# Kernel tuning notes

Hardware: AMD Instinct MI355X
Metric: run time of the kernel (lower is better)

Reference implementation:

```python
import jax, jax.numpy as jnp
import numpy as np

T = 1.0        # temperature (init kwarg t)
NEG = -1e9     # finite mask value: exp(NEG - max) underflows to exactly 0 in fp32


def setup_inputs() -> dict:
    key = jax.random.key(0)
    k1, k2 = jax.random.split(key)
    B, L, D = 48, 17, 256
    x = jax.random.normal(k1, (B, L, D), dtype=jnp.float32)
    label = jax.random.randint(k2, (B,), 0, 8, dtype=jnp.int64)
    return {"input": x, "label": label}


def _loss(x, label):
    B, L, D = x.shape
    M = B * (L - 1)
    # F.normalize(dim=2)
    xn = x / jnp.maximum(jnp.linalg.norm(x, axis=2, keepdims=True), 1e-12)
    anchors = xn[:, 0]                         # [B, D]
    toks = xn[:, 1:].reshape(M, D)             # [M, D], row r belongs to sample owner[r]
    owner = jnp.repeat(jnp.arange(B), L - 1)   # [M]
    same = label[:, None] == label[owner][None, :]   # [B, M] same-class mask per anchor
    neg = ~same                                      # negative-column mask per anchor

    s_anc = (anchors @ toks.T) / T   # [B, M] anchor-vs-token scores
    s_tok = (toks @ toks.T) / T      # [M, M] token-vs-token scores

    # anchor_consistent_score_unify: softmax of s_anc over negative columns only
    a_logits = jnp.where(neg, s_anc, NEG)                       # [B, M]
    log_denom = jax.scipy.special.logsumexp(a_logits, axis=1)   # [B]  log sum_c exp(s_anc)
    a_unify = jnp.exp(a_logits - log_denom[:, None])            # [B, M], 0 at masked cols
    # positive_consistent_score_unify: exp(s_tok) / anchor denom (NOT a row softmax)
    p_unify = jnp.exp(s_tok[None, :, :] - log_denom[:, None, None])  # [B, M, M]

    # second-level Softmax / LogSoftmax applied to the unify VALUES, neg cols only
    a_m = jnp.where(neg, a_unify, NEG)                 # [B, M]
    p_m = jnp.where(neg[:, None, :], p_unify, NEG)     # [B, M, M]
    log_a = jax.nn.log_softmax(a_m, axis=1)            # [B, M]
    log_p = jax.nn.log_softmax(p_m, axis=2)            # [B, M, M]
    sm_a = jnp.exp(log_a)
    sm_p = jnp.exp(log_p)

    col = neg[:, None, :]
    # KL(input=log_a repeated over rows, target=sm_p), elementwise t*(log t - inp)
    kl1 = jnp.where(col, sm_p * (log_p - log_a[:, None, :]), 0.0).sum(axis=2)          # [B, M]
    # KL(input=log_p, target=sm_a repeated over rows)
    kl2 = jnp.where(col, sm_a[:, None, :] * (log_a[:, None, :] - log_p), 0.0).sum(axis=2)

    row = same.astype(x.dtype)              # positive rows for anchor i
    P = row.sum(axis=1)                     # batchmean divisor = #positive rows
    l1 = (kl1 * row).sum(axis=1) / P
    l2 = (kl2 * row).sum(axis=1) / P
    return jnp.mean(0.5 * l1 + 0.5 * l2)


def reference(input, label):
    return _loss(input, label)
```

## Files before the change

### kernel.cpp

```cpp
#include <hip/hip_runtime.h>
#include <math.h>

#define Bn 48
#define Ln 17
#define Dn 256
#define Mn 768
#define NS 2
#define LDA 76

static __device__ __forceinline__ double pexp(double e) {
  return 1.0 + e*(1.0 + e*(0.5 + e*((1.0/6.0) + e*((1.0/24.0) + e*(1.0/120.0)))));
}

static __device__ __forceinline__ double blockReduce16(double v, double* red) {
  __syncthreads();
  #pragma unroll
  for (int o = 32; o > 0; o >>= 1) v += __shfl_down(v, o, 64);
  int lane = threadIdx.x & 63, wid = threadIdx.x >> 6;
  if (lane == 0) red[wid] = v;
  __syncthreads();
  double r = 0.0;
  #pragma unroll
  for (int w = 0; w < 16; ++w) r += red[w];
  return r;
}

static __device__ __forceinline__ int src_row_m(int m) {
  if (m < Bn) return m * Ln;
  int t = m - Bn;
  return (t >> 4) * Ln + (t & 15) + 1;
}
static __device__ __forceinline__ int src_row_n(int n) {
  return (n >> 4) * Ln + (n & 15) + 1;
}

__global__ __launch_bounds__(256) void kA_gemm(const float* __restrict__ x,
                                               double* __restrict__ EA,
                                               double* __restrict__ E,
                                               float* __restrict__ out) {
  __shared__ float As[16][LDA];
  __shared__ float Bs[16][LDA];
  __shared__ float nA[64], nB[64];
  int tid = threadIdx.x;
  if (blockIdx.x == 0 && blockIdx.y == 0 && tid == 0) out[0] = 0.f;
  int m0 = blockIdx.y * 64, n0 = blockIdx.x * 64;
  int r  = tid >> 2, cq = tid & 3;
  int mrow = m0 + r;
  int gm = (mrow < 816) ? src_row_m(mrow) : 0;
  int gn = src_row_n(n0 + r);
  const float* pa = x + gm * Dn + cq * 4;
  const float* pb = x + gn * Dn + cq * 4;
  float4 ra = *(const float4*)pa;
  float4 rb = *(const float4*)pb;
  float ssa = 0.f, ssb = 0.f;
  float c[4][4];
  #pragma unroll
  for (int i = 0; i < 4; ++i)
    #pragma unroll
    for (int j = 0; j < 4; ++j) c[i][j] = 0.f;
  int tx = tid & 15, ty = tid >> 4;

  for (int t = 0; t < 16; ++t) {
    __syncthreads();
    int kb = cq * 4;
    As[kb+0][r] = ra.x; As[kb+1][r] = ra.y; As[kb+2][r] = ra.z; As[kb+3][r] = ra.w;
    Bs[kb+0][r] = rb.x; Bs[kb+1][r] = rb.y; Bs[kb+2][r] = rb.z; Bs[kb+3][r] = rb.w;
    ssa += ra.x*ra.x + ra.y*ra.y + ra.z*ra.z + ra.w*ra.w;
    ssb += rb.x*rb.x + rb.y*rb.y + rb.z*rb.z + rb.w*rb.w;
    __syncthreads();
    if (t < 15) {
      ra = *(const float4*)(pa + (t + 1) * 16);
      rb = *(const float4*)(pb + (t + 1) * 16);
    }
    #pragma unroll
    for (int k = 0; k < 16; ++k) {
      float4 a4 = *(const float4*)&As[k][ty * 4];
      float4 b4 = *(const float4*)&Bs[k][tx * 4];
      float av[4] = {a4.x, a4.y, a4.z, a4.w};
      float bv[4] = {b4.x, b4.y, b4.z, b4.w};
      #pragma unroll
      for (int i = 0; i < 4; ++i)
        #pragma unroll
        for (int j = 0; j < 4; ++j) c[i][j] = fmaf(av[i], bv[j], c[i][j]);
    }
  }
  ssa += __shfl_xor(ssa, 1, 64); ssa += __shfl_xor(ssa, 2, 64);
  ssb += __shfl_xor(ssb, 1, 64); ssb += __shfl_xor(ssb, 2, 64);
  if (cq == 0) { nA[r] = ssa; nB[r] = ssb; }
  __syncthreads();
  double ia[4], ib[4];
  #pragma unroll
  for (int i = 0; i < 4; ++i) ia[i] = 1.0 / sqrt((double)nA[ty * 4 + i]);
  #pragma unroll
  for (int j = 0; j < 4; ++j) ib[j] = 1.0 / sqrt((double)nB[tx * 4 + j]);
  #pragma unroll
  for (int i = 0; i < 4; ++i) {
    int m = m0 + ty * 4 + i;
    if (m >= 816) continue;
    #pragma unroll
    for (int j = 0; j < 4; ++j) {
      int n = n0 + tx * 4 + j;
      double ev = exp((double)c[i][j] * ia[i] * ib[j]);
      if (m < Bn) EA[m * Mn + n] = ev;
      else        E[(m - Bn) * Mn + n] = ev;
    }
  }
}

__global__ __launch_bounds__(1024, 2) void kB_i(const double* __restrict__ EA,
                                                const double* __restrict__ E,
                                                const int* __restrict__ label,
                                                float* __restrict__ out) {
  __shared__ double2 sp[Mn];
  __shared__ double red[16];
  __shared__ int lab[Bn];
  int slice = blockIdx.x, i = blockIdx.y;
  int tid = threadIdx.x;
  int lane = tid & 63, w = tid >> 6;
  if (tid < Bn) lab[tid] = label[tid];
  __syncthreads();
  int li = lab[i];

  bool has = (tid < Mn);
  bool neg = has && (lab[tid >> 4] != li);
  double eav = has ? EA[i * Mn + tid] : 0.0;
  double s1 = blockReduce16(neg ? eav : 0.0, red);
  double ci = 1.0 / s1;
  double a = ci * eav;
  double p = pexp(a);
  if (has) { sp[tid].x = neg ? a : 0.0; sp[tid].y = neg ? p : 0.0; }
  double t2a = blockReduce16(neg ? p : 0.0, red);
  double t2b = blockReduce16(neg ? p * a : 0.0, red);
  double inv_s2 = 1.0 / t2a;
  double Evi = t2b * inv_s2;
  unsigned long long nm = __ballot(lane < Bn && lab[lane] != li);
  int cnt = 64 - __popcll(nm | 0xFFFF000000000000ull);

  int kb0 = lane >> 4;
  double tsum = 0.0;
  for (int bj = slice; bj < Bn; bj += NS) {
    if (lab[bj] != li) continue;
    const double* Ej = E + (bj * 16 + w) * Mn + lane;
    double Evv[12];
    #pragma unroll
    for (int it = 0; it < 12; ++it) Evv[it] = Ej[64 * it];
    double A = 0.0, Bv = 0.0, C = 0.0, D2 = 0.0;
    #pragma unroll
    for (int it = 0; it < 12; ++it) {
      double m = (double)((nm >> (kb0 + 4 * it)) & 1ull);
      double e = ci * Evv[it];
      double wx = pexp(e);
      double wm = wx * m;
      double2 s = sp[lane + 64 * it];
      A  = fma(wm, e, A);
      Bv = fma(wx, s.x, Bv);
      C += wm;
      D2 = fma(s.y, e, D2);
    }
    #pragma unroll
    for (int o = 32; o > 0; o >>= 1) {
      A  += __shfl_xor(A,  o, 64);
      Bv += __shfl_xor(Bv, o, 64);
      C  += __shfl_xor(C,  o, 64);
      D2 += __shfl_xor(D2, o, 64);
    }
    tsum += (A - Bv) / C - D2 * inv_s2 + Evi;
  }

  __syncthreads();
  if (lane == 0) red[w] = tsum;
  __syncthreads();
  if (tid == 0) {
    double s = 0.0;
    #pragma unroll
    for (int ww = 0; ww < 16; ++ww) s += red[ww];
    atomicAdd(out, (float)(s / (1536.0 * (double)cnt)));
  }
}

extern "C" void kernel_launch(void* const* d_in, const int* in_sizes, int n_in,
                              void* d_out, int out_size, void* d_ws, size_t ws_size,
                              hipStream_t stream) {
  const float* x   = (const float*)d_in[0];
  const int* label = (const int*)d_in[1];
  float* out = (float*)d_out;

  char* ws = (char*)d_ws;
  size_t off = 0;
  auto alloc = [&](size_t bytes) -> void* {
    void* p = ws + off;
    off = (off + bytes + 255) & ~(size_t)255;
    return p;
  };
  double* EA = (double*)alloc((size_t)Bn * Mn * sizeof(double));
  double* E  = (double*)alloc((size_t)Mn * Mn * sizeof(double));

  kA_gemm<<<dim3(12, 13), 256, 0, stream>>>(x, EA, E, out);
  kB_i<<<dim3(NS, Bn), 1024, 0, stream>>>(EA, E, label, out);
}
```

Baseline: 91.92 us.

## Fuse GEMM and loss kernels into one cooperative launch with grid sync

Merges the score/exp GEMM kernel and the per-anchor KL reduction kernel into a single cooperative kernel of 1024-thread blocks. A grid-wide sync separates the two phases, and only the first 96 blocks continue into the reduction. The GEMM phase now gives each thread a 2x2 output tile, but only 256 threads do the loads. This removes one kernel launch and its inter-kernel gap. The cost is a grid barrier, a smaller per-thread tile, idle loader threads, and a reduction phase that may run at lower occupancy.

```diff
diff --git a/kernel.cpp b/kernel.cpp
--- a/kernel.cpp
+++ b/kernel.cpp
@@ -1,12 +1,16 @@
 #include <hip/hip_runtime.h>
+#include <hip/hip_cooperative_groups.h>
 #include <math.h>
+
+namespace cg = cooperative_groups;
 
 #define Bn 48
 #define Ln 17
 #define Dn 256
 #define Mn 768
-#define NS 2
 #define LDA 76
+#define NBLK 156
+#define NKB 96
 
 static __device__ __forceinline__ double pexp(double e) {
   return 1.0 + e*(1.0 + e*(0.5 + e*((1.0/6.0) + e*((1.0/24.0) + e*(1.0/120.0)))));
@@ -34,88 +38,100 @@
   return (n >> 4) * Ln + (n & 15) + 1;
 }
 
-__global__ __launch_bounds__(256) void kA_gemm(const float* __restrict__ x,
+__global__ __launch_bounds__(1024) void kFused(const float* __restrict__ x,
+                                               const int* __restrict__ label,
                                                double* __restrict__ EA,
                                                double* __restrict__ E,
                                                float* __restrict__ out) {
-  __shared__ float As[16][LDA];
-  __shared__ float Bs[16][LDA];
-  __shared__ float nA[64], nB[64];
-  int tid = threadIdx.x;
-  if (blockIdx.x == 0 && blockIdx.y == 0 && tid == 0) out[0] = 0.f;
-  int m0 = blockIdx.y * 64, n0 = blockIdx.x * 64;
-  int r  = tid >> 2, cq = tid & 3;
-  int mrow = m0 + r;
-  int gm = (mrow < 816) ? src_row_m(mrow) : 0;
-  int gn = src_row_n(n0 + r);
-  const float* pa = x + gm * Dn + cq * 4;
-  const float* pb = x + gn * Dn + cq * 4;
-  float4 ra = *(const float4*)pa;
-  float4 rb = *(const float4*)pb;
-  float ssa = 0.f, ssb = 0.f;
-  float c[4][4];
-  #pragma unroll
-  for (int i = 0; i < 4; ++i)
-    #pragma unroll
-    for (int j = 0; j < 4; ++j) c[i][j] = 0.f;
-  int tx = tid & 15, ty = tid >> 4;
-
-  for (int t = 0; t < 16; ++t) {
-    __syncthreads();
-    int kb = cq * 4;
-    As[kb+0][r] = ra.x; As[kb+1][r] = ra.y; As[kb+2][r] = ra.z; As[kb+3][r] = ra.w;
-    Bs[kb+0][r] = rb.x; Bs[kb+1][r] = rb.y; Bs[kb+2][r] = rb.z; Bs[kb+3][r] = rb.w;
-    ssa += ra.x*ra.x + ra.y*ra.y + ra.z*ra.z + ra.w*ra.w;
-    ssb += rb.x*rb.x + rb.y*rb.y + rb.z*rb.z + rb.w*rb.w;
-    __syncthreads();
-    if (t < 15) {
-      ra = *(const float4*)(pa + (t + 1) * 16);
-      rb = *(const float4*)(pb + (t + 1) * 16);
-    }
-    #pragma unroll
-    for (int k = 0; k < 16; ++k) {
-      float4 a4 = *(const float4*)&As[k][ty * 4];
-      float4 b4 = *(const float4*)&Bs[k][tx * 4];
-      float av[4] = {a4.x, a4.y, a4.z, a4.w};
-      float bv[4] = {b4.x, b4.y, b4.z, b4.w};
-      #pragma unroll
-      for (int i = 0; i < 4; ++i)
-        #pragma unroll
-        for (int j = 0; j < 4; ++j) c[i][j] = fmaf(av[i], bv[j], c[i][j]);
-    }
-  }
-  ssa += __shfl_xor(ssa, 1, 64); ssa += __shfl_xor(ssa, 2, 64);
-  ssb += __shfl_xor(ssb, 1, 64); ssb += __shfl_xor(ssb, 2, 64);
-  if (cq == 0) { nA[r] = ssa; nB[r] = ssb; }
-  __syncthreads();
-  double ia[4], ib[4];
-  #pragma unroll
-  for (int i = 0; i < 4; ++i) ia[i] = 1.0 / sqrt((double)nA[ty * 4 + i]);
-  #pragma unroll
-  for (int j = 0; j < 4; ++j) ib[j] = 1.0 / sqrt((double)nB[tx * 4 + j]);
-  #pragma unroll
-  for (int i = 0; i < 4; ++i) {
-    int m = m0 + ty * 4 + i;
-    if (m >= 816) continue;
-    #pragma unroll
-    for (int j = 0; j < 4; ++j) {
-      int n = n0 + tx * 4 + j;
-      double ev = exp((double)c[i][j] * ia[i] * ib[j]);
-      if (m < Bn) EA[m * Mn + n] = ev;
-      else        E[(m - Bn) * Mn + n] = ev;
-    }
-  }
-}
-
-__global__ __launch_bounds__(1024, 2) void kB_i(const double* __restrict__ EA,
-                                                const double* __restrict__ E,
-                                                const int* __restrict__ label,
-                                                float* __restrict__ out) {
   __shared__ double2 sp[Mn];
   __shared__ double red[16];
   __shared__ int lab[Bn];
-  int slice = blockIdx.x, i = blockIdx.y;
+
   int tid = threadIdx.x;
+  int blk = blockIdx.x;
+
+  {
+    float* As = (float*)sp;
+    float* Bs = As + 16 * LDA;
+    float* nA = Bs + 16 * LDA;
+    float* nB = nA + 64;
+
+    if (blk == 0 && tid == 0) out[0] = 0.f;
+    int tn = blk % 12, tm = blk / 12;
+    int m0 = tm * 64, n0 = tn * 64;
+
+    int r = tid >> 2, cq = tid & 3;
+    const float* pa = x;
+    const float* pb = x;
+    float4 ra = {0,0,0,0}, rb = {0,0,0,0};
+    if (tid < 256) {
+      int mrow = m0 + r;
+      int gm = (mrow < 816) ? src_row_m(mrow) : 0;
+      int gn = src_row_n(n0 + r);
+      pa = x + gm * Dn + cq * 4;
+      pb = x + gn * Dn + cq * 4;
+      ra = *(const float4*)pa;
+      rb = *(const float4*)pb;
+    }
+    float ssa = 0.f, ssb = 0.f;
+    float c00 = 0.f, c01 = 0.f, c10 = 0.f, c11 = 0.f;
+    int tx = tid & 31, ty = tid >> 5;
+
+    for (int t = 0; t < 16; ++t) {
+      __syncthreads();
+      if (tid < 256) {
+        int kb = cq * 4;
+        As[(kb+0)*LDA + r] = ra.x; As[(kb+1)*LDA + r] = ra.y;
+        As[(kb+2)*LDA + r] = ra.z; As[(kb+3)*LDA + r] = ra.w;
+        Bs[(kb+0)*LDA + r] = rb.x; Bs[(kb+1)*LDA + r] = rb.y;
+        Bs[(kb+2)*LDA + r] = rb.z; Bs[(kb+3)*LDA + r] = rb.w;
+        ssa += ra.x*ra.x + ra.y*ra.y + ra.z*ra.z + ra.w*ra.w;
+        ssb += rb.x*rb.x + rb.y*rb.y + rb.z*rb.z + rb.w*rb.w;
+      }
+      __syncthreads();
+      if (tid < 256 && t < 15) {
+        ra = *(const float4*)(pa + (t + 1) * 16);
+        rb = *(const float4*)(pb + (t + 1) * 16);
+      }
+      #pragma unroll
+      for (int k = 0; k < 16; ++k) {
+        float a0 = As[k*LDA + ty*2], a1 = As[k*LDA + ty*2 + 1];
+        float b0 = Bs[k*LDA + tx*2], b1 = Bs[k*LDA + tx*2 + 1];
+        c00 = fmaf(a0, b0, c00); c01 = fmaf(a0, b1, c01);
+        c10 = fmaf(a1, b0, c10); c11 = fmaf(a1, b1, c11);
+      }
+    }
+    if (tid < 256) {
+      ssa += __shfl_xor(ssa, 1, 64); ssa += __shfl_xor(ssa, 2, 64);
+      ssb += __shfl_xor(ssb, 1, 64); ssb += __shfl_xor(ssb, 2, 64);
+      if (cq == 0) { nA[r] = ssa; nB[r] = ssb; }
+    }
+    __syncthreads();
+    double ia0 = 1.0 / sqrt((double)nA[ty*2]);
+    double ia1 = 1.0 / sqrt((double)nA[ty*2 + 1]);
+    double ib0 = 1.0 / sqrt((double)nB[tx*2]);
+    double ib1 = 1.0 / sqrt((double)nB[tx*2 + 1]);
+    float cv[2][2] = {{c00, c01}, {c10, c11}};
+    double iav[2] = {ia0, ia1}, ibv[2] = {ib0, ib1};
+    #pragma unroll
+    for (int i2 = 0; i2 < 2; ++i2) {
+      int m = m0 + ty*2 + i2;
+      if (m >= 816) continue;
+      #pragma unroll
+      for (int j2 = 0; j2 < 2; ++j2) {
+        int n = n0 + tx*2 + j2;
+        double ev = exp((double)cv[i2][j2] * iav[i2] * ibv[j2]);
+        if (m < Bn) EA[m * Mn + n] = ev;
+        else        E[(m - Bn) * Mn + n] = ev;
+      }
+    }
+  }
+
+  cg::this_grid().sync();
+
+  if (blk >= NKB) return;
+
+  int slice = blk & 1, i = blk >> 1;
   int lane = tid & 63, w = tid >> 6;
   if (tid < Bn) lab[tid] = label[tid];
   __syncthreads();
@@ -138,7 +154,7 @@
 
   int kb0 = lane >> 4;
   double tsum = 0.0;
-  for (int bj = slice; bj < Bn; bj += NS) {
+  for (int bj = slice; bj < Bn; bj += 2) {
     if (lab[bj] != li) continue;
     const double* Ej = E + (bj * 16 + w) * Mn + lane;
     double Evv[12];
@@ -195,6 +211,7 @@
   double* EA = (double*)alloc((size_t)Bn * Mn * sizeof(double));
   double* E  = (double*)alloc((size_t)Mn * Mn * sizeof(double));
 
-  kA_gemm<<<dim3(12, 13), 256, 0, stream>>>(x, EA, E, out);
-  kB_i<<<dim3(NS, Bn), 1024, 0, stream>>>(EA, E, label, out);
-}
+  void* args[] = {(void*)&x, (void*)&label, (void*)&EA, (void*)&E, (void*)&out};
+  hipLaunchCooperativeKernel((const void*)kFused, dim3(NBLK), dim3(1024),
+                             args, 0, stream);
+}
```

After: 133.6 us. +45.4%, slower.

## Fuse GEMM and loss kernels into one cooperative launch with grid sync

Applied to the files above, without the earlier changes.

Merges the score/exp GEMM kernel and the per-anchor KL reduction kernel into a single cooperative kernel of 240 blocks of 256 threads. The first 156 blocks compute the GEMM tiles, then a grid-wide sync separates the phases. In the second phase each block handles one anchor and one of 5 slices, and each wave processes 4 token rows instead of one. This removes a kernel launch boundary and raises parallelism in the second phase, at the cost of a grid-sync barrier, idle blocks during the GEMM phase, and more serial work per wave.

```diff
diff --git a/kernel.cpp b/kernel.cpp
--- a/kernel.cpp
+++ b/kernel.cpp
@@ -1,28 +1,30 @@
 #include <hip/hip_runtime.h>
+#include <hip/hip_cooperative_groups.h>
 #include <math.h>
+
+namespace cg = cooperative_groups;
 
 #define Bn 48
 #define Ln 17
 #define Dn 256
 #define Mn 768
-#define NS 2
 #define LDA 76
+#define NTILE 156
+#define NS 5
+#define NBLK 240
 
 static __device__ __forceinline__ double pexp(double e) {
   return 1.0 + e*(1.0 + e*(0.5 + e*((1.0/6.0) + e*((1.0/24.0) + e*(1.0/120.0)))));
 }
 
-static __device__ __forceinline__ double blockReduce16(double v, double* red) {
+static __device__ __forceinline__ double bRed4(double v, double* red) {
   __syncthreads();
   #pragma unroll
   for (int o = 32; o > 0; o >>= 1) v += __shfl_down(v, o, 64);
   int lane = threadIdx.x & 63, wid = threadIdx.x >> 6;
   if (lane == 0) red[wid] = v;
   __syncthreads();
-  double r = 0.0;
-  #pragma unroll
-  for (int w = 0; w < 16; ++w) r += red[w];
-  return r;
+  return red[0] + red[1] + red[2] + red[3];
 }
 
 static __device__ __forceinline__ int src_row_m(int m) {
@@ -34,103 +36,121 @@
   return (n >> 4) * Ln + (n & 15) + 1;
 }
 
-__global__ __launch_bounds__(256) void kA_gemm(const float* __restrict__ x,
-                                               double* __restrict__ EA,
-                                               double* __restrict__ E,
-                                               float* __restrict__ out) {
+__global__ __launch_bounds__(256) void kFused(const float* __restrict__ x,
+                                              const int* __restrict__ label,
+                                              double* __restrict__ EA,
+                                              double* __restrict__ E,
+                                              float* __restrict__ out) {
   __shared__ float As[16][LDA];
   __shared__ float Bs[16][LDA];
   __shared__ float nA[64], nB[64];
+  __shared__ double2 sp[Mn];
+  __shared__ double red[4];
+  __shared__ int lab[Bn];
+
   int tid = threadIdx.x;
-  if (blockIdx.x == 0 && blockIdx.y == 0 && tid == 0) out[0] = 0.f;
-  int m0 = blockIdx.y * 64, n0 = blockIdx.x * 64;
-  int r  = tid >> 2, cq = tid & 3;
-  int mrow = m0 + r;
-  int gm = (mrow < 816) ? src_row_m(mrow) : 0;
-  int gn = src_row_n(n0 + r);
-  const float* pa = x + gm * Dn + cq * 4;
-  const float* pb = x + gn * Dn + cq * 4;
-  float4 ra = *(const float4*)pa;
-  float4 rb = *(const float4*)pb;
-  float ssa = 0.f, ssb = 0.f;
-  float c[4][4];
-  #pragma unroll
-  for (int i = 0; i < 4; ++i)
-    #pragma unroll
-    for (int j = 0; j < 4; ++j) c[i][j] = 0.f;
-  int tx = tid & 15, ty = tid >> 4;
-
-  for (int t = 0; t < 16; ++t) {
+  int blk = blockIdx.x;
+
+  if (blk < NTILE) {
+    if (blk == 0 && tid == 0) out[0] = 0.f;
+    int tn = blk % 12, tm = blk / 12;
+    int m0 = tm * 64, n0 = tn * 64;
+    int r  = tid >> 2, cq = tid & 3;
+    int mrow = m0 + r;
+    int gm = (mrow < 816) ? src_row_m(mrow) : 0;
+    int gn = src_row_n(n0 + r);
+    const float* pa = x + gm * Dn + cq * 4;
+    const float* pb = x + gn * Dn + cq * 4;
+    float4 ra = *(const float4*)pa;
+    float4 rb = *(const float4*)pb;
+    float ssa = 0.f, ssb = 0.f;
+    float c[4][4];
+    #pragma unroll
+    for (int i = 0; i < 4; ++i)
+      #pragma unroll
+      for (int j = 0; j < 4; ++j) c[i][j] = 0.f;
+    int tx = tid & 15, ty = tid >> 4;
+
+    for (int t = 0; t < 16; ++t) {
+      __syncthreads();
+      int kb = cq * 4;
+      As[kb+0][r] = ra.x; As[kb+1][r] = ra.y; As[kb+2][r] = ra.z; As[kb+3][r] = ra.w;
+      Bs[kb+0][r] = rb.x; Bs[kb+1][r] = rb.y; Bs[kb+2][r] = rb.z; Bs[kb+3][r] = rb.w;
+      ssa += ra.x*ra.x + ra.y*ra.y + ra.z*ra.z + ra.w*ra.w;
+      ssb += rb.x*rb.x + rb.y*rb.y + rb.z*rb.z + rb.w*rb.w;
+      __syncthreads();
+      if (t < 15) {
+        ra = *(const float4*)(pa + (t + 1) * 16);
+        rb = *(const float4*)(pb + (t + 1) * 16);
+      }
+      #pragma unroll
+      for (int k = 0; k < 16; ++k) {
+        float4 a4 = *(const float4*)&As[k][ty * 4];
+        float4 b4 = *(const float4*)&Bs[k][tx * 4];
+        float av[4] = {a4.x, a4.y, a4.z, a4.w};
+        float bv[4] = {b4.x, b4.y, b4.z, b4.w};
+        #pragma unroll
+        for (int i = 0; i < 4; ++i)
+          #pragma unroll
+          for (int j = 0; j < 4; ++j) c[i][j] = fmaf(av[i], bv[j], c[i][j]);
+      }
+    }
+    ssa += __shfl_xor(ssa, 1, 64); ssa += __shfl_xor(ssa, 2, 64);
+    ssb += __shfl_xor(ssb, 1, 64); ssb += __shfl_xor(ssb, 2, 64);
+    if (cq == 0) { nA[r] = ssa; nB[r] = ssb; }
     __syncthreads();
-    int kb = cq * 4;
-    As[kb+0][r] = ra.x; As[kb+1][r] = ra.y; As[kb+2][r] = ra.z; As[kb+3][r] = ra.w;
-    Bs[kb+0][r] = rb.x; Bs[kb+1][r] = rb.y; Bs[kb+2][r] = rb.z; Bs[kb+3][r] = rb.w;
-    ssa += ra.x*ra.x + ra.y*ra.y + ra.z*ra.z + ra.w*ra.w;
-    ssb += rb.x*rb.x + rb.y*rb.y + rb.z*rb.z + rb.w*rb.w;
-    __syncthreads();
-    if (t < 15) {
-      ra = *(const float4*)(pa + (t + 1) * 16);
-      rb = *(const float4*)(pb + (t + 1) * 16);
+    double ia[4], ib[4];
+    #pragma unroll
+    for (int i = 0; i < 4; ++i) ia[i] = 1.0 / sqrt((double)nA[ty * 4 + i]);
+    #pragma unroll
+    for (int j = 0; j < 4; ++j) ib[j] = 1.0 / sqrt((double)nB[tx * 4 + j]);
+    #pragma unroll
+    for (int i = 0; i < 4; ++i) {
+      int m = m0 + ty * 4 + i;
+      if (m < 816) {
+        #pragma unroll
+        for (int j = 0; j < 4; ++j) {
+          int n = n0 + tx * 4 + j;
+          double ev = exp((double)c[i][j] * ia[i] * ib[j]);
+          if (m < Bn) EA[m * Mn + n] = ev;
+          else        E[(m - Bn) * Mn + n] = ev;
+        }
+      }
     }
-    #pragma unroll
-    for (int k = 0; k < 16; ++k) {
-      float4 a4 = *(const float4*)&As[k][ty * 4];
-      float4 b4 = *(const float4*)&Bs[k][tx * 4];
-      float av[4] = {a4.x, a4.y, a4.z, a4.w};
-      float bv[4] = {b4.x, b4.y, b4.z, b4.w};
-      #pragma unroll
-      for (int i = 0; i < 4; ++i)
-        #pragma unroll
-        for (int j = 0; j < 4; ++j) c[i][j] = fmaf(av[i], bv[j], c[i][j]);
-    }
-  }
-  ssa += __shfl_xor(ssa, 1, 64); ssa += __shfl_xor(ssa, 2, 64);
-  ssb += __shfl_xor(ssb, 1, 64); ssb += __shfl_xor(ssb, 2, 64);
-  if (cq == 0) { nA[r] = ssa; nB[r] = ssb; }
-  __syncthreads();
-  double ia[4], ib[4];
-  #pragma unroll
-  for (int i = 0; i < 4; ++i) ia[i] = 1.0 / sqrt((double)nA[ty * 4 + i]);
-  #pragma unroll
-  for (int j = 0; j < 4; ++j) ib[j] = 1.0 / sqrt((double)nB[tx * 4 + j]);
-  #pragma unroll
-  for (int i = 0; i < 4; ++i) {
-    int m = m0 + ty * 4 + i;
-    if (m >= 816) continue;
-    #pragma unroll
-    for (int j = 0; j < 4; ++j) {
-      int n = n0 + tx * 4 + j;
-      double ev = exp((double)c[i][j] * ia[i] * ib[j]);
-      if (m < Bn) EA[m * Mn + n] = ev;
-      else        E[(m - Bn) * Mn + n] = ev;
-    }
-  }
-}
-
-__global__ __launch_bounds__(1024, 2) void kB_i(const double* __restrict__ EA,
-                                                const double* __restrict__ E,
-                                                const int* __restrict__ label,
-                                                float* __restrict__ out) {
-  __shared__ double2 sp[Mn];
-  __shared__ double red[16];
-  __shared__ int lab[Bn];
-  int slice = blockIdx.x, i = blockIdx.y;
-  int tid = threadIdx.x;
+  }
+
+  cg::this_grid().sync();
+
+  int slice = blk / Bn, i = blk % Bn;
   int lane = tid & 63, w = tid >> 6;
   if (tid < Bn) lab[tid] = label[tid];
   __syncthreads();
   int li = lab[i];
 
-  bool has = (tid < Mn);
-  bool neg = has && (lab[tid >> 4] != li);
-  double eav = has ? EA[i * Mn + tid] : 0.0;
-  double s1 = blockReduce16(neg ? eav : 0.0, red);
+  double ev3[3];
+  bool ng3[3];
+  double s1l = 0.0;
+  #pragma unroll
+  for (int rr = 0; rr < 3; ++rr) {
+    int k = tid + 256 * rr;
+    ng3[rr] = (lab[k >> 4] != li);
+    ev3[rr] = EA[i * Mn + k];
+    if (ng3[rr]) s1l += ev3[rr];
+  }
+  double s1 = bRed4(s1l, red);
   double ci = 1.0 / s1;
-  double a = ci * eav;
-  double p = pexp(a);
-  if (has) { sp[tid].x = neg ? a : 0.0; sp[tid].y = neg ? p : 0.0; }
-  double t2a = blockReduce16(neg ? p : 0.0, red);
-  double t2b = blockReduce16(neg ? p * a : 0.0, red);
+  double t2al = 0.0, t2bl = 0.0;
+  #pragma unroll
+  for (int rr = 0; rr < 3; ++rr) {
+    int k = tid + 256 * rr;
+    double a = ci * ev3[rr];
+    double p = pexp(a);
+    sp[k].x = ng3[rr] ? a : 0.0;
+    sp[k].y = ng3[rr] ? p : 0.0;
+    if (ng3[rr]) { t2al += p; t2bl += p * a; }
+  }
+  double t2a = bRed4(t2al, red);
+  double t2b = bRed4(t2bl, red);
   double inv_s2 = 1.0 / t2a;
   double Evi = t2b * inv_s2;
   unsigned long long nm = __ballot(lane < Bn && lab[lane] != li);
@@ -140,40 +160,42 @@
   double tsum = 0.0;
   for (int bj = slice; bj < Bn; bj += NS) {
     if (lab[bj] != li) continue;
-    const double* Ej = E + (bj * 16 + w) * Mn + lane;
-    double Evv[12];
-    #pragma unroll
-    for (int it = 0; it < 12; ++it) Evv[it] = Ej[64 * it];
-    double A = 0.0, Bv = 0.0, C = 0.0, D2 = 0.0;
-    #pragma unroll
-    for (int it = 0; it < 12; ++it) {
-      double m = (double)((nm >> (kb0 + 4 * it)) & 1ull);
-      double e = ci * Evv[it];
-      double wx = pexp(e);
-      double wm = wx * m;
-      double2 s = sp[lane + 64 * it];
-      A  = fma(wm, e, A);
-      Bv = fma(wx, s.x, Bv);
-      C += wm;
-      D2 = fma(s.y, e, D2);
+    #pragma unroll
+    for (int jj = 0; jj < 4; ++jj) {
+      int j = bj * 16 + w * 4 + jj;
+      const double* Ej = E + j * Mn + lane;
+      double Evv[12];
+      #pragma unroll
+      for (int it = 0; it < 12; ++it) Evv[it] = Ej[64 * it];
+      double A = 0.0, Bv = 0.0, C = 0.0, D2 = 0.0;
+      #pragma unroll
+      for (int it = 0; it < 12; ++it) {
+        double m = (double)((nm >> (kb0 + 4 * it)) & 1ull);
+        double e = ci * Evv[it];
+        double wx = pexp(e);
+        double wm = wx * m;
+        double2 s = sp[lane + 64 * it];
+        A  = fma(wm, e, A);
+        Bv = fma(wx, s.x, Bv);
+        C += wm;
+        D2 = fma(s.y, e, D2);
+      }
+      #pragma unroll
+      for (int o = 32; o > 0; o >>= 1) {
+        A  += __shfl_xor(A,  o, 64);
+        Bv += __shfl_xor(Bv, o, 64);
+        C  += __shfl_xor(C,  o, 64);
+        D2 += __shfl_xor(D2, o, 64);
+      }
+      tsum += (A - Bv) / C - D2 * inv_s2 + Evi;
     }
-    #pragma unroll
-    for (int o = 32; o > 0; o >>= 1) {
-      A  += __shfl_xor(A,  o, 64);
-      Bv += __shfl_xor(Bv, o, 64);
-      C  += __shfl_xor(C,  o, 64);
-      D2 += __shfl_xor(D2, o, 64);
-    }
-    tsum += (A - Bv) / C - D2 * inv_s2 + Evi;
   }
 
   __syncthreads();
   if (lane == 0) red[w] = tsum;
   __syncthreads();
   if (tid == 0) {
-    double s = 0.0;
-    #pragma unroll
-    for (int ww = 0; ww < 16; ++ww) s += red[ww];
+    double s = red[0] + red[1] + red[2] + red[3];
     atomicAdd(out, (float)(s / (1536.0 * (double)cnt)));
   }
 }
@@ -195,6 +217,7 @@
   double* EA = (double*)alloc((size_t)Bn * Mn * sizeof(double));
   double* E  = (double*)alloc((size_t)Mn * Mn * sizeof(double));
 
-  kA_gemm<<<dim3(12, 13), 256, 0, stream>>>(x, EA, E, out);
-  kB_i<<<dim3(NS, Bn), 1024, 0, stream>>>(EA, E, label, out);
-}
+  void* args[] = {(void*)&x, (void*)&label, (void*)&EA, (void*)&E, (void*)&out};
+  hipLaunchCooperativeKernel((const void*)kFused, dim3(NBLK), dim3(256),
+                             args, 0, stream);
+}
```

New measurement: 131.0 us. 42.5% more time.
